# Performance work log

Measured on AMD Instinct MI355X. Metric: run time of the kernel, lower is better.

The kernel has to match this reference:

```python
import jax, jax.numpy as jnp
import numpy as np

DIM = 768
B, N = 8, 2048


def setup_inputs() -> dict:
    key = jax.random.key(0)
    k = jax.random.split(key, 8)
    s = 1.0 / np.sqrt(DIM)
    return {
        "x": jax.random.normal(k[0], (B, N, DIM), jnp.float32),
        "x2": jax.random.normal(k[1], (B, N, DIM), jnp.float32),
        "x3": jax.random.normal(k[2], (B, N, DIM), jnp.float32),
        "W1": jax.random.uniform(k[3], (DIM, DIM), jnp.float32, -s, s),
        "b1": jax.random.uniform(k[4], (DIM,), jnp.float32, -s, s),
        "W2": jax.random.uniform(k[5], (DIM, DIM), jnp.float32, -s, s),
        "b2": jax.random.uniform(k[6], (DIM,), jnp.float32, -s, s),
        "w": jnp.ones((1,), jnp.float32),
    }


def _cross_attention(x, x2, W, b):
    # key = softmax(x2.transpose(1,2), dim=1) -> softmax over feature axis, then [B, D, N]
    key = jnp.swapaxes(jax.nn.softmax(x2, axis=-1), 1, 2)  # [B, D, N]
    query = jax.nn.softmax(x2, axis=1)                      # [B, N, D], softmax over tokens
    context = jnp.einsum('bnd,bdm->bnm', x, key)            # [B, N, N]
    atten = jnp.einsum('bnm,bmd->bnd', context, query)      # [B, N, D]
    return atten @ W.T + b


def reference(x, x2, x3, W1, b1, W2, b2, w):
    a1 = _cross_attention(x, x2, W1, b1)
    a2 = _cross_attention(x, x3, W2, b2)
    f = jax.nn.sigmoid(w)  # scalar gate, broadcast
    atten = a1 * f + a2 * f
    return atten + x
```

## Files before the change

kernel.cpp:

```cpp
#include <hip/hip_runtime.h>

#define DIMD 768
#define NTOK 2048
#define NB   8

typedef __attribute__((ext_vector_type(8))) short bfrag8;
typedef __attribute__((ext_vector_type(4))) float accf4;

__device__ __forceinline__ unsigned short f2bf(float f) {
  unsigned u = __float_as_uint(f);
  return (unsigned short)((u + 0x7fffu + ((u >> 16) & 1u)) >> 16);
}

__device__ __forceinline__ void glds16(const void* g, void* l) {
  __builtin_amdgcn_global_load_lds(
      (const __attribute__((address_space(1))) void*)g,
      (__attribute__((address_space(3))) void*)l, 16, 0, 0);
}


__device__ __forceinline__ void packw_body(int blk, const float* __restrict__ W1,
                                           const float* __restrict__ W2,
                                           unsigned short* __restrict__ Wcat) {
  int gid = blk * 256 + threadIdx.x;
  int r = gid / 192, c4 = (gid % 192) * 4;
  float4 a = *(const float4*)(W1 + (size_t)r * DIMD + c4);
  float4 b = *(const float4*)(W2 + (size_t)r * DIMD + c4);
  union { unsigned short us[4]; uint2 u2; } ra, rb;
  ra.us[0] = f2bf(a.x); ra.us[1] = f2bf(a.y); ra.us[2] = f2bf(a.z); ra.us[3] = f2bf(a.w);
  rb.us[0] = f2bf(b.x); rb.us[1] = f2bf(b.y); rb.us[2] = f2bf(b.z); rb.us[3] = f2bf(b.w);
  *(uint2*)(Wcat + (size_t)r * 1536 + c4) = ra.u2;
  *(uint2*)(Wcat + (size_t)r * 1536 + 768 + c4) = rb.u2;
}

__device__ __forceinline__ void packx_body(int blk, const float* __restrict__ x,
                                           unsigned short* __restrict__ xb) {
  size_t gid = (size_t)blk * 256 + threadIdx.x;
  const float4* x4 = (const float4*)x;
  float4 v0 = x4[gid * 2], v1 = x4[gid * 2 + 1];
  union { unsigned short us[8]; uint4 u4; } r;
  r.us[0] = f2bf(v0.x); r.us[1] = f2bf(v0.y); r.us[2] = f2bf(v0.z); r.us[3] = f2bf(v0.w);
  r.us[4] = f2bf(v1.x); r.us[5] = f2bf(v1.y); r.us[6] = f2bf(v1.z); r.us[7] = f2bf(v1.w);
  ((uint4*)xb)[gid] = r.u4;
}

template <int TMD, int TND, int EPI>
__device__ __forceinline__ void gemm_body(
    unsigned short* As, unsigned short* Bs, int bid,
    const unsigned short* __restrict__ A, const unsigned short* __restrict__ B,
    void* __restrict__ Cout, int K, int lda, int ldb, int ldc, int ntx,
    long long sA, long long sB, long long sC,
    const float* __restrict__ wg, const float* __restrict__ b1v,
    const float* __restrict__ b2v, const float* __restrict__ xres) {
  constexpr int TM = 64 * TMD, TN = 64 * TND;
  constexpr int ASZ = TM * 64, BSZ = TN * 64;
  __shared__ float csi[64 * TND];
  const int t = threadIdx.x, w = t >> 6, lane = t & 63;
  const int bz = bid & 7;
  const int r = bid >> 3;
  const int by = r / ntx, bx = r - by * ntx;
  const int m0 = by * TM, n0 = bx * TN;
  const unsigned short* Ab = A + (size_t)bz * sA;
  const unsigned short* Bb = B + (size_t)bz * sB;
  const int srow = lane >> 3;
  const int scol = (((lane & 7) ^ (lane >> 3)) * 8);

  auto stage = [&](int buf, int k0) {
    unsigned short* Ad = As + buf * ASZ;
    unsigned short* Bd = Bs + buf * BSZ;
#pragma unroll
    for (int l = 0; l < 2 * TND; ++l) {
      int chunk = l * 4 + w;
      int row = chunk * 8 + srow;
      glds16(Bb + (size_t)(n0 + row) * ldb + k0 + scol,
             (char*)Bd + chunk * 1024 + lane * 16);
    }
#pragma unroll
    for (int l = 0; l < 2 * TMD; ++l) {
      int chunk = l * 4 + w;
      int row = chunk * 8 + srow;
      glds16(Ab + (size_t)(m0 + row) * lda + k0 + scol,
             (char*)Ad + chunk * 1024 + lane * 16);
    }
  };

  stage(0, 0);

  if (EPI == 2) {
    for (int c = t; c < TN; c += 256) {
      const float* cp = b1v + (size_t)bz * 32 * DIMD + n0 + c;
      float s = 0.f;
#pragma unroll
      for (int p = 0; p < 32; ++p) s += cp[(size_t)p * DIMD];
      csi[c] = 1.0f / s;
    }
  }

  accf4 zero = {0.f, 0.f, 0.f, 0.f};
  accf4 acc[2 * TMD][2 * TND];
#pragma unroll
  for (int i = 0; i < 2 * TMD; ++i)
#pragma unroll
    for (int j = 0; j < 2 * TND; ++j) acc[i][j] = zero;

  const int wm = (w & 1) * (32 * TMD), wn = (w >> 1) * (32 * TND);
  const int lm = lane & 15, qd = lane >> 4;
  const int lsw = (lm & 7) << 3;

  __syncthreads();

  const int nt = K / 64;
  int cur = 0;
#pragma unroll 2
  for (int tt = 0; tt < nt; ++tt) {
    if (tt + 1 < nt) stage(cur ^ 1, (tt + 1) * 64);
    const unsigned short* Ar = As + cur * ASZ;
    const unsigned short* Br = Bs + cur * BSZ;
#pragma unroll
    for (int kc = 0; kc < 2; ++kc) {
      bfrag8 av[2 * TMD], bv[2 * TND];
      const int kslot = (((kc << 2) | qd) << 3) ^ lsw;
#pragma unroll
      for (int i = 0; i < 2 * TMD; ++i)
        av[i] = *(const bfrag8*)(Ar + (wm + i * 16 + lm) * 64 + kslot);
#pragma unroll
      for (int j = 0; j < 2 * TND; ++j)
        bv[j] = *(const bfrag8*)(Br + (wn + j * 16 + lm) * 64 + kslot);
      __builtin_amdgcn_s_setprio(1);
#pragma unroll
      for (int i = 0; i < 2 * TMD; ++i)
#pragma unroll
        for (int j = 0; j < 2 * TND; ++j)
          acc[i][j] = __builtin_amdgcn_mfma_f32_16x16x32_bf16(av[i], bv[j], acc[i][j], 0, 0, 0);
      __builtin_amdgcn_s_setprio(0);
    }
    if (tt + 1 < nt) {
      asm volatile("s_waitcnt vmcnt(0)\n\ts_barrier" ::: "memory");
    }
    cur ^= 1;
  }

  if (EPI == 0) {
    unsigned short* Cb = (unsigned short*)Cout + (size_t)bz * sC;
#pragma unroll
    for (int i = 0; i < 2 * TMD; ++i)
#pragma unroll
      for (int j = 0; j < 2 * TND; ++j) {
        int col = n0 + wn + j * 16 + lm;
#pragma unroll
        for (int rr = 0; rr < 4; ++rr) {
          int row = m0 + wm + i * 16 + qd * 4 + rr;
          Cb[(size_t)row * ldc + col] = f2bf(acc[i][j][rr]);
        }
      }
  } else if (EPI == 1) {
    float gate = 1.f / (1.f + __expf(-wg[0]));
    float* Co = (float*)Cout + (size_t)bz * sC;
    const float* Xr = xres + (size_t)bz * sC;
#pragma unroll
    for (int j = 0; j < 2 * TND; ++j) {
      int col = n0 + wn + j * 16 + lm;
      float gb = gate * (b1v[col] + b2v[col]);
#pragma unroll
      for (int i = 0; i < 2 * TMD; ++i)
#pragma unroll
        for (int rr = 0; rr < 4; ++rr) {
          int row = m0 + wm + i * 16 + qd * 4 + rr;
          size_t idx = (size_t)row * ldc + col;
          Co[idx] = gate * acc[i][j][rr] + gb + Xr[idx];
        }
    }
  } else {
    unsigned short* Cb = (unsigned short*)Cout + (size_t)bz * sC;
#pragma unroll
    for (int j = 0; j < 2 * TND; ++j) {
      int lc = wn + j * 16 + lm;
      int col = n0 + lc;
      float ci = csi[lc];
#pragma unroll
      for (int i = 0; i < 2 * TMD; ++i)
#pragma unroll
        for (int rr = 0; rr < 4; ++rr) {
          int row = m0 + wm + i * 16 + qd * 4 + rr;
          Cb[(size_t)row * ldc + col] = f2bf(acc[i][j][rr] * ci);
        }
    }
  }
}

__global__ __launch_bounds__(256) void stage1_kernel(
    const float* __restrict__ xA, unsigned short* __restrict__ KtA,
    unsigned short* __restrict__ QtA, float* __restrict__ cspA,
    const float* __restrict__ xB, unsigned short* __restrict__ KtB,
    unsigned short* __restrict__ QtB, float* __restrict__ cspB,
    int nsm,
    const float* __restrict__ W1, const float* __restrict__ W2,
    unsigned short* __restrict__ Wcat, int npw) {
  int blk = blockIdx.x;
  if (blk >= nsm) {
    if (blk < nsm + npw) packw_body(blk - nsm, W1, W2, Wcat);
    return;
  }
  __shared__ float rowsi[64];
  __shared__ __align__(16) unsigned short etile[768 * 72];
  const int sel = blk >> 8;
  const float* xin = sel ? xB : xA;
  unsigned short* Kt = sel ? KtB : KtA;
  unsigned short* Qt = sel ? QtB : QtA;
  float* csp = sel ? cspB : cspA;
  const int lb = blk & 255;
  const int b = (lb >> 5) & 7, ntile = lb & 31, n0 = ntile * 64;
  const int t = threadIdx.x;

  const int tok = t >> 2, seg = t & 3;
  const float* row = xin + ((size_t)b * NTOK + n0 + tok) * DIMD + seg * 192;
  float s = 0.f;
#pragma unroll 12
  for (int j = 0; j < 48; ++j) {
    float4 v = *(const float4*)(row + j * 4);
    float e0 = __expf(v.x), e1 = __expf(v.y), e2 = __expf(v.z), e3 = __expf(v.w);
    s += (e0 + e1) + (e2 + e3);
    int d = seg * 192 + j * 4;
    etile[(d + 0) * 72 + tok] = f2bf(e0);
    etile[(d + 1) * 72 + tok] = f2bf(e1);
    etile[(d + 2) * 72 + tok] = f2bf(e2);
    etile[(d + 3) * 72 + tok] = f2bf(e3);
  }
  s += __shfl_xor(s, 1, 64);
  s += __shfl_xor(s, 2, 64);
  if (seg == 0) rowsi[tok] = 1.0f / s;
  __syncthreads();

#pragma unroll 4
  for (int q = 0; q < 24; ++q) {
    int dl = (t >> 3) + q * 32;
    int g = t & 7;
    uint4 e8 = *(const uint4*)(etile + dl * 72 + g * 8);
    float ef[8];
    ef[0] = __uint_as_float(e8.x << 16); ef[1] = __uint_as_float(e8.x & 0xffff0000u);
    ef[2] = __uint_as_float(e8.y << 16); ef[3] = __uint_as_float(e8.y & 0xffff0000u);
    ef[4] = __uint_as_float(e8.z << 16); ef[5] = __uint_as_float(e8.z & 0xffff0000u);
    ef[6] = __uint_as_float(e8.w << 16); ef[7] = __uint_as_float(e8.w & 0xffff0000u);
    float4 r0 = *(const float4*)&rowsi[g * 8];
    float4 r1 = *(const float4*)&rowsi[g * 8 + 4];
    union { unsigned short us[8]; uint4 u4; } ko;
    ko.us[0] = f2bf(ef[0] * r0.x); ko.us[1] = f2bf(ef[1] * r0.y);
    ko.us[2] = f2bf(ef[2] * r0.z); ko.us[3] = f2bf(ef[3] * r0.w);
    ko.us[4] = f2bf(ef[4] * r1.x); ko.us[5] = f2bf(ef[5] * r1.y);
    ko.us[6] = f2bf(ef[6] * r1.z); ko.us[7] = f2bf(ef[7] * r1.w);
    size_t orow = ((size_t)b * DIMD + dl) * NTOK + n0 + g * 8;
    *(uint4*)(Kt + orow) = ko.u4;
    *(uint4*)(Qt + orow) = e8;
    float cs = ((ef[0] + ef[1]) + (ef[2] + ef[3])) + ((ef[4] + ef[5]) + (ef[6] + ef[7]));
    cs += __shfl_xor(cs, 1, 64);
    cs += __shfl_xor(cs, 2, 64);
    cs += __shfl_xor(cs, 4, 64);
    if (g == 0) csp[((size_t)b * 32 + ntile) * DIMD + dl] = cs;
  }
}

template <int TMD, int TND, int EPI>
__global__ __launch_bounds__(256) void mfma_bt(
    const unsigned short* __restrict__ A, const unsigned short* __restrict__ B,
    void* __restrict__ Cout, int K, int lda, int ldb, int ldc, int ntx,
    long long sA, long long sB, long long sC,
    const float* __restrict__ wg, const float* __restrict__ b1v,
    const float* __restrict__ b2v, const float* __restrict__ xres) {
  __shared__ __align__(16) unsigned short As[2 * 64 * TMD * 64];
  __shared__ __align__(16) unsigned short Bs[2 * 64 * TND * 64];
  gemm_body<TMD, TND, EPI>(As, Bs, blockIdx.x, A, B, Cout, K, lda, ldb, ldc, ntx,
                           sA, sB, sC, wg, b1v, b2v, xres);
}

__global__ __launch_bounds__(256) void sgemm_s(
    const unsigned short* __restrict__ KtA, const unsigned short* __restrict__ QtA,
    const float* __restrict__ cspA,
    const unsigned short* __restrict__ KtB, const unsigned short* __restrict__ QtB,
    const float* __restrict__ cspB,
    unsigned short* __restrict__ Ca, unsigned short* __restrict__ Cb) {
  __shared__ __align__(16) unsigned short As[2 * 128 * 64];
  __shared__ __align__(16) unsigned short Bs[2 * 128 * 64];
  bool second = blockIdx.x >= 288;
  const unsigned short* A = second ? KtB : KtA;
  const unsigned short* B = second ? QtB : QtA;
  const float* csp = second ? cspB : cspA;
  unsigned short* C = second ? Cb : Ca;
  int blk = second ? (blockIdx.x - 288) : blockIdx.x;
  gemm_body<2, 2, 2>(As, Bs, blk, A, B, C, NTOK, NTOK, NTOK, 1536, 6,
                     768LL * NTOK, 768LL * NTOK, 768LL * 1536,
                     nullptr, csp, nullptr, nullptr);
}

__global__ __launch_bounds__(256) void s2_packx_kernel(
    const unsigned short* __restrict__ Wcat, const unsigned short* __restrict__ Scat,
    unsigned short* __restrict__ Bt, const float* __restrict__ x,
    unsigned short* __restrict__ xb) {
  __shared__ __align__(16) unsigned short As[2 * 128 * 64];
  __shared__ __align__(16) unsigned short Bs[2 * 128 * 64];
  int blk = blockIdx.x;
  if (blk < 288) {
    gemm_body<2, 2, 0>(As, Bs, blk, Wcat, Scat, Bt, 1536, 1536, 1536, 768, 6,
                       0LL, 768LL * 1536, 768LL * 768,
                       nullptr, nullptr, nullptr, nullptr);
  } else {
    packx_body(blk - 288, x, xb);
  }
}

extern "C" void kernel_launch(void* const* d_in, const int* in_sizes, int n_in,
                              void* d_out, int out_size, void* d_ws, size_t ws_size,
                              hipStream_t stream) {
  const float* x  = (const float*)d_in[0];
  const float* x2 = (const float*)d_in[1];
  const float* x3 = (const float*)d_in[2];
  const float* W1 = (const float*)d_in[3];
  const float* b1 = (const float*)d_in[4];
  const float* W2 = (const float*)d_in[5];
  const float* b2 = (const float*)d_in[6];
  const float* w  = (const float*)d_in[7];
  float* out = (float*)d_out;
  char* ws = (char*)d_ws;

  dim3 blk(256);
  const bool merged = ws_size >= 123600896ull;

  if (merged) {
    unsigned short* Kt1  = (unsigned short*)(ws + 0);
    unsigned short* Qt1  = (unsigned short*)(ws + 25165824);
    unsigned short* Kt2  = (unsigned short*)(ws + 50331648);
    unsigned short* Qt2  = (unsigned short*)(ws + 75497472);
    unsigned short* Scat = (unsigned short*)(ws + 100663296);
    unsigned short* Wcat = (unsigned short*)(ws + 119537664);
    float* csp1 = (float*)(ws + 121896960);
    float* csp2 = (float*)(ws + 122683392);
    unsigned short* Bt = (unsigned short*)(ws + 0);
    unsigned short* xb = (unsigned short*)(ws + 9437184);

    stage1_kernel<<<1088, blk, 0, stream>>>(x2, Kt1, Qt1, csp1,
                                            x3, Kt2, Qt2, csp2, 512,
                                            W1, W2, Wcat, 576);
    sgemm_s<<<576, blk, 0, stream>>>(Kt1, Qt1, csp1, Kt2, Qt2, csp2, Scat, Scat + 768);
    s2_packx_kernel<<<6432, blk, 0, stream>>>(Wcat, Scat, Bt, x, xb);
    mfma_bt<2, 2, 1><<<768, blk, 0, stream>>>(xb, Bt, out, DIMD, DIMD, DIMD, DIMD, 6,
                                              (long long)NTOK * DIMD, 768LL * 768,
                                              (long long)NTOK * DIMD, w, b1, b2, x);
  } else {
    unsigned short* Kt   = (unsigned short*)(ws + 0);
    unsigned short* Qt   = (unsigned short*)(ws + 25165824);
    unsigned short* Scat = (unsigned short*)(ws + 50331648);
    unsigned short* Bt   = (unsigned short*)(ws + 69206016);
    float* csp1 = (float*)(ws + 69206016);
    float* csp2 = (float*)(ws + 69992448);
    unsigned short* xb   = (unsigned short*)(ws + 78643200);
    unsigned short* Wcat = (unsigned short*)(ws + 103809024);

    stage1_kernel<<<832, blk, 0, stream>>>(x2, Kt, Qt, csp1,
                                           x2, Kt, Qt, csp1, 256,
                                           W1, W2, Wcat, 576);
    sgemm_s<<<288, blk, 0, stream>>>(Kt, Qt, csp1, Kt, Qt, csp1, Scat, Scat);
    stage1_kernel<<<256, blk, 0, stream>>>(x3, Kt, Qt, csp2,
                                           x3, Kt, Qt, csp2, 256,
                                           W1, W2, Wcat, 0);
    sgemm_s<<<288, blk, 0, stream>>>(Kt, Qt, csp2, Kt, Qt, csp2, Scat + 768, Scat + 768);
    s2_packx_kernel<<<6432, blk, 0, stream>>>(Wcat, Scat, Bt, x, xb);
    mfma_bt<2, 2, 1><<<768, blk, 0, stream>>>(xb, Bt, out, DIMD, DIMD, DIMD, DIMD, 6,
                                              (long long)NTOK * DIMD, 768LL * 768,
                                              (long long)NTOK * DIMD, w, b1, b2, x);
  }
}
```

Baseline: 323.0 us.

## Use symmetric sqrt row-scaled feature matrix for both GEMM operands

```diff
diff --git a/kernel.cpp b/kernel.cpp
--- a/kernel.cpp
+++ b/kernel.cpp
@@ -88,10 +88,10 @@
 
   if (EPI == 2) {
     for (int c = t; c < TN; c += 256) {
-      const float* cp = b1v + (size_t)bz * 32 * DIMD + n0 + c;
+      const float* cp = b1v + (size_t)bz * 64 * DIMD + n0 + c;
       float s = 0.f;
 #pragma unroll
-      for (int p = 0; p < 32; ++p) s += cp[(size_t)p * DIMD];
+      for (int p = 0; p < 64; ++p) s += cp[(size_t)p * DIMD];
       csi[c] = 1.0f / s;
     }
   }
@@ -188,74 +188,91 @@
   }
 }
 
-__global__ __launch_bounds__(256) void stage1_kernel(
-    const float* __restrict__ xA, unsigned short* __restrict__ KtA,
-    unsigned short* __restrict__ QtA, float* __restrict__ cspA,
-    const float* __restrict__ xB, unsigned short* __restrict__ KtB,
-    unsigned short* __restrict__ QtB, float* __restrict__ cspB,
-    int nsm,
+__global__ __launch_bounds__(256) void rowcol_kernel(
+    const float* __restrict__ x2, const float* __restrict__ x3,
+    float* __restrict__ csp1, float* __restrict__ csp2,
+    float* __restrict__ rsf,
     const float* __restrict__ W1, const float* __restrict__ W2,
     unsigned short* __restrict__ Wcat, int npw) {
   int blk = blockIdx.x;
-  if (blk >= nsm) {
-    if (blk < nsm + npw) packw_body(blk - nsm, W1, W2, Wcat);
+  if (blk >= 1024) {
+    if (blk < 1024 + npw) packw_body(blk - 1024, W1, W2, Wcat);
     return;
   }
-  __shared__ float rowsi[64];
-  __shared__ __align__(16) unsigned short etile[768 * 72];
-  const int sel = blk >> 8;
-  const float* xin = sel ? xB : xA;
-  unsigned short* Kt = sel ? KtB : KtA;
-  unsigned short* Qt = sel ? QtB : QtA;
-  float* csp = sel ? cspB : cspA;
-  const int lb = blk & 255;
-  const int b = (lb >> 5) & 7, ntile = lb & 31, n0 = ntile * 64;
+  const int sel = blk >> 9, b = (blk >> 6) & 7, tile = blk & 63;
+  const float* xin = sel ? x3 : x2;
+  float* csp = sel ? csp2 : csp1;
+  float* rso = rsf + (size_t)sel * NB * NTOK + (size_t)b * NTOK + tile * 32;
+  const float* xb_ = xin + ((size_t)b * NTOK + tile * 32) * DIMD;
+  const int t = threadIdx.x, w = t >> 6, lane = t & 63;
+  __shared__ float cred[4][DIMD];
+
+  const int d0 = lane * 12;
+  float cs[12];
+#pragma unroll
+  for (int i = 0; i < 12; ++i) cs[i] = 0.f;
+
+#pragma unroll
+  for (int v = 0; v < 8; ++v) {
+    int tok = w * 8 + v;
+    const float* row = xb_ + (size_t)tok * DIMD + d0;
+    float4 a = *(const float4*)(row);
+    float4 c = *(const float4*)(row + 4);
+    float4 d = *(const float4*)(row + 8);
+    float e[12];
+    e[0] = __expf(a.x); e[1] = __expf(a.y); e[2] = __expf(a.z); e[3] = __expf(a.w);
+    e[4] = __expf(c.x); e[5] = __expf(c.y); e[6] = __expf(c.z); e[7] = __expf(c.w);
+    e[8] = __expf(d.x); e[9] = __expf(d.y); e[10] = __expf(d.z); e[11] = __expf(d.w);
+    float rp = 0.f;
+#pragma unroll
+    for (int i = 0; i < 12; ++i) { rp += e[i]; cs[i] += e[i]; }
+#pragma unroll
+    for (int off = 32; off; off >>= 1) rp += __shfl_xor(rp, off, 64);
+    if (lane == 0) rso[tok] = sqrtf(1.0f / rp);
+  }
+#pragma unroll
+  for (int i = 0; i < 12; ++i) cred[w][d0 + i] = cs[i];
+  __syncthreads();
+#pragma unroll
+  for (int i = 0; i < 3; ++i) {
+    int d = t * 3 + i;
+    float s = cred[0][d] + cred[1][d] + cred[2][d] + cred[3][d];
+    csp[((size_t)b * 64 + tile) * DIMD + d] = s;
+  }
+}
+
+__global__ __launch_bounds__(256) void ft_kernel(
+    const float* __restrict__ x2, const float* __restrict__ x3,
+    const float* __restrict__ rsf,
+    unsigned short* __restrict__ Ft1, unsigned short* __restrict__ Ft2) {
+  __shared__ __align__(16) unsigned short etile[192 * 72];
+  const int blk = blockIdx.x;
+  const int sel = blk >> 10, lb = blk & 1023;
+  const int b = lb >> 7, rr = lb & 127, ntile = rr >> 2, dc = rr & 3;
+  const float* xin = sel ? x3 : x2;
+  unsigned short* Ft = sel ? Ft2 : Ft1;
+  const float* rsv = rsf + (size_t)sel * NB * NTOK + (size_t)b * NTOK + ntile * 64;
   const int t = threadIdx.x;
 
-  const int tok = t >> 2, seg = t & 3;
-  const float* row = xin + ((size_t)b * NTOK + n0 + tok) * DIMD + seg * 192;
-  float s = 0.f;
-#pragma unroll 12
-  for (int j = 0; j < 48; ++j) {
+  const int tok = t >> 2, q4 = t & 3;
+  const float* row = xin + ((size_t)b * NTOK + ntile * 64 + tok) * DIMD + dc * 192 + q4 * 48;
+  const float fsc = rsv[tok];
+#pragma unroll
+  for (int j = 0; j < 12; ++j) {
     float4 v = *(const float4*)(row + j * 4);
-    float e0 = __expf(v.x), e1 = __expf(v.y), e2 = __expf(v.z), e3 = __expf(v.w);
-    s += (e0 + e1) + (e2 + e3);
-    int d = seg * 192 + j * 4;
-    etile[(d + 0) * 72 + tok] = f2bf(e0);
-    etile[(d + 1) * 72 + tok] = f2bf(e1);
-    etile[(d + 2) * 72 + tok] = f2bf(e2);
-    etile[(d + 3) * 72 + tok] = f2bf(e3);
-  }
-  s += __shfl_xor(s, 1, 64);
-  s += __shfl_xor(s, 2, 64);
-  if (seg == 0) rowsi[tok] = 1.0f / s;
+    int dl = q4 * 48 + j * 4;
+    etile[(dl + 0) * 72 + tok] = f2bf(__expf(v.x) * fsc);
+    etile[(dl + 1) * 72 + tok] = f2bf(__expf(v.y) * fsc);
+    etile[(dl + 2) * 72 + tok] = f2bf(__expf(v.z) * fsc);
+    etile[(dl + 3) * 72 + tok] = f2bf(__expf(v.w) * fsc);
+  }
   __syncthreads();
-
-#pragma unroll 4
-  for (int q = 0; q < 24; ++q) {
-    int dl = (t >> 3) + q * 32;
+#pragma unroll
+  for (int k = 0; k < 6; ++k) {
+    int dl = (t >> 3) + k * 32;
     int g = t & 7;
     uint4 e8 = *(const uint4*)(etile + dl * 72 + g * 8);
-    float ef[8];
-    ef[0] = __uint_as_float(e8.x << 16); ef[1] = __uint_as_float(e8.x & 0xffff0000u);
-    ef[2] = __uint_as_float(e8.y << 16); ef[3] = __uint_as_float(e8.y & 0xffff0000u);
-    ef[4] = __uint_as_float(e8.z << 16); ef[5] = __uint_as_float(e8.z & 0xffff0000u);
-    ef[6] = __uint_as_float(e8.w << 16); ef[7] = __uint_as_float(e8.w & 0xffff0000u);
-    float4 r0 = *(const float4*)&rowsi[g * 8];
-    float4 r1 = *(const float4*)&rowsi[g * 8 + 4];
-    union { unsigned short us[8]; uint4 u4; } ko;
-    ko.us[0] = f2bf(ef[0] * r0.x); ko.us[1] = f2bf(ef[1] * r0.y);
-    ko.us[2] = f2bf(ef[2] * r0.z); ko.us[3] = f2bf(ef[3] * r0.w);
-    ko.us[4] = f2bf(ef[4] * r1.x); ko.us[5] = f2bf(ef[5] * r1.y);
-    ko.us[6] = f2bf(ef[6] * r1.z); ko.us[7] = f2bf(ef[7] * r1.w);
-    size_t orow = ((size_t)b * DIMD + dl) * NTOK + n0 + g * 8;
-    *(uint4*)(Kt + orow) = ko.u4;
-    *(uint4*)(Qt + orow) = e8;
-    float cs = ((ef[0] + ef[1]) + (ef[2] + ef[3])) + ((ef[4] + ef[5]) + (ef[6] + ef[7]));
-    cs += __shfl_xor(cs, 1, 64);
-    cs += __shfl_xor(cs, 2, 64);
-    cs += __shfl_xor(cs, 4, 64);
-    if (g == 0) csp[((size_t)b * 32 + ntile) * DIMD + dl] = cs;
+    *(uint4*)(Ft + ((size_t)b * DIMD + dc * 192 + dl) * NTOK + ntile * 64 + g * 8) = e8;
   }
 }
 
@@ -273,20 +290,17 @@
 }
 
 __global__ __launch_bounds__(256) void sgemm_s(
-    const unsigned short* __restrict__ KtA, const unsigned short* __restrict__ QtA,
-    const float* __restrict__ cspA,
-    const unsigned short* __restrict__ KtB, const unsigned short* __restrict__ QtB,
-    const float* __restrict__ cspB,
+    const unsigned short* __restrict__ Ft1, const float* __restrict__ csp1,
+    const unsigned short* __restrict__ Ft2, const float* __restrict__ csp2,
     unsigned short* __restrict__ Ca, unsigned short* __restrict__ Cb) {
   __shared__ __align__(16) unsigned short As[2 * 128 * 64];
   __shared__ __align__(16) unsigned short Bs[2 * 128 * 64];
   bool second = blockIdx.x >= 288;
-  const unsigned short* A = second ? KtB : KtA;
-  const unsigned short* B = second ? QtB : QtA;
-  const float* csp = second ? cspB : cspA;
+  const unsigned short* F = second ? Ft2 : Ft1;
+  const float* csp = second ? csp2 : csp1;
   unsigned short* C = second ? Cb : Ca;
   int blk = second ? (blockIdx.x - 288) : blockIdx.x;
-  gemm_body<2, 2, 2>(As, Bs, blk, A, B, C, NTOK, NTOK, NTOK, 1536, 6,
+  gemm_body<2, 2, 2>(As, Bs, blk, F, F, C, NTOK, NTOK, NTOK, 1536, 6,
                      768LL * NTOK, 768LL * NTOK, 768LL * 1536,
                      nullptr, csp, nullptr, nullptr);
 }
@@ -321,50 +335,23 @@
   float* out = (float*)d_out;
   char* ws = (char*)d_ws;
 
+  unsigned short* Ft1  = (unsigned short*)(ws + 0);
+  unsigned short* Ft2  = (unsigned short*)(ws + 25165824);
+  unsigned short* Scat = (unsigned short*)(ws + 50331648);
+  unsigned short* Wcat = (unsigned short*)(ws + 69206016);
+  float* csp1 = (float*)(ws + 71565312);
+  float* csp2 = (float*)(ws + 73138176);
+  float* rsf  = (float*)(ws + 74711040);
+  unsigned short* Bt = (unsigned short*)(ws + 0);
+  unsigned short* xb = (unsigned short*)(ws + 9437184);
+
   dim3 blk(256);
-  const bool merged = ws_size >= 123600896ull;
-
-  if (merged) {
-    unsigned short* Kt1  = (unsigned short*)(ws + 0);
-    unsigned short* Qt1  = (unsigned short*)(ws + 25165824);
-    unsigned short* Kt2  = (unsigned short*)(ws + 50331648);
-    unsigned short* Qt2  = (unsigned short*)(ws + 75497472);
-    unsigned short* Scat = (unsigned short*)(ws + 100663296);
-    unsigned short* Wcat = (unsigned short*)(ws + 119537664);
-    float* csp1 = (float*)(ws + 121896960);
-    float* csp2 = (float*)(ws + 122683392);
-    unsigned short* Bt = (unsigned short*)(ws + 0);
-    unsigned short* xb = (unsigned short*)(ws + 9437184);
-
-    stage1_kernel<<<1088, blk, 0, stream>>>(x2, Kt1, Qt1, csp1,
-                                            x3, Kt2, Qt2, csp2, 512,
-                                            W1, W2, Wcat, 576);
-    sgemm_s<<<576, blk, 0, stream>>>(Kt1, Qt1, csp1, Kt2, Qt2, csp2, Scat, Scat + 768);
-    s2_packx_kernel<<<6432, blk, 0, stream>>>(Wcat, Scat, Bt, x, xb);
-    mfma_bt<2, 2, 1><<<768, blk, 0, stream>>>(xb, Bt, out, DIMD, DIMD, DIMD, DIMD, 6,
-                                              (long long)NTOK * DIMD, 768LL * 768,
-                                              (long long)NTOK * DIMD, w, b1, b2, x);
-  } else {
-    unsigned short* Kt   = (unsigned short*)(ws + 0);
-    unsigned short* Qt   = (unsigned short*)(ws + 25165824);
-    unsigned short* Scat = (unsigned short*)(ws + 50331648);
-    unsigned short* Bt   = (unsigned short*)(ws + 69206016);
-    float* csp1 = (float*)(ws + 69206016);
-    float* csp2 = (float*)(ws + 69992448);
-    unsigned short* xb   = (unsigned short*)(ws + 78643200);
-    unsigned short* Wcat = (unsigned short*)(ws + 103809024);
-
-    stage1_kernel<<<832, blk, 0, stream>>>(x2, Kt, Qt, csp1,
-                                           x2, Kt, Qt, csp1, 256,
-                                           W1, W2, Wcat, 576);
-    sgemm_s<<<288, blk, 0, stream>>>(Kt, Qt, csp1, Kt, Qt, csp1, Scat, Scat);
-    stage1_kernel<<<256, blk, 0, stream>>>(x3, Kt, Qt, csp2,
-                                           x3, Kt, Qt, csp2, 256,
-                                           W1, W2, Wcat, 0);
-    sgemm_s<<<288, blk, 0, stream>>>(Kt, Qt, csp2, Kt, Qt, csp2, Scat + 768, Scat + 768);
-    s2_packx_kernel<<<6432, blk, 0, stream>>>(Wcat, Scat, Bt, x, xb);
-    mfma_bt<2, 2, 1><<<768, blk, 0, stream>>>(xb, Bt, out, DIMD, DIMD, DIMD, DIMD, 6,
-                                              (long long)NTOK * DIMD, 768LL * 768,
-                                              (long long)NTOK * DIMD, w, b1, b2, x);
-  }
-}
+
+  rowcol_kernel<<<1600, blk, 0, stream>>>(x2, x3, csp1, csp2, rsf, W1, W2, Wcat, 576);
+  ft_kernel<<<2048, blk, 0, stream>>>(x2, x3, rsf, Ft1, Ft2);
+  sgemm_s<<<576, blk, 0, stream>>>(Ft1, csp1, Ft2, csp2, Scat, Scat + 768);
+  s2_packx_kernel<<<6432, blk, 0, stream>>>(Wcat, Scat, Bt, x, xb);
+  mfma_bt<2, 2, 1><<<768, blk, 0, stream>>>(xb, Bt, out, DIMD, DIMD, DIMD, DIMD, 6,
+                                            (long long)NTOK * DIMD, 768LL * 768,
+                                            (long long)NTOK * DIMD, w, b1, b2, x);
+}
```

New measurement: 328.0 us. About the same (+1.6%).
